# Performance work log

Hardware: AMD Instinct MI355X
Metric: run time of the kernel (lower is better)

## Reference

```python
import jax, jax.numpy as jnp
import numpy as np

B, T, D_IN, D_OUT = 32, 2048, 512, 512


def setup_inputs() -> dict:
    key = jax.random.key(0)
    k1, k2, k3 = jax.random.split(key, 3)
    x = jax.random.normal(k1, (B, T, D_IN), dtype=jnp.float32)
    # scale weights roughly like glorot / orthogonal init
    W = jax.random.normal(k2, (D_IN, D_OUT), dtype=jnp.float32) * (1.0 / np.sqrt(D_IN))
    W_recurrent = jax.random.normal(k3, (D_OUT, D_OUT), dtype=jnp.float32) * (1.0 / np.sqrt(D_OUT))
    b = jnp.zeros((D_OUT,), dtype=jnp.float32)
    return {"x": x, "W": W, "W_recurrent": W_recurrent, "b": b}


def reference(x, W, W_recurrent, b):
    # x: [B, T, D_in]. Vanilla RNN: h_t = tanh(x_t @ W + h_{t-1} @ W_rec + b)
    # Precompute input projections for all timesteps in one big GEMM,
    # then scan only the recurrent part (same math as per-step matmul).
    xw = jnp.einsum('bti,io->tbo', x, W) + b  # [T, B, D_out]
    h0 = jnp.zeros((x.shape[0], W.shape[1]), dtype=x.dtype)

    def step(h, xw_t):
        h_new = jnp.tanh(xw_t + h @ W_recurrent)
        return h_new, h_new

    _, states = jax.lax.scan(step, h0, xw)  # states: [T, B, D_out]
    # return_sequence=True -> [B, T, D_out]
    return jnp.transpose(states, (1, 0, 2))
```

## Files before the change

kernel.cpp:

```cpp
#include <hip/hip_runtime.h>

constexpr int B = 32, T = 2048, D = 512;

typedef float f32x4 __attribute__((ext_vector_type(4)));

__global__ __launch_bounds__(256) void xw_gemm(
    const float* __restrict__ A, const float* __restrict__ W,
    const float* __restrict__ bias, float* __restrict__ C) {
  __shared__ float As[16][68];
  __shared__ float Bs[16][68];
  const int tid = threadIdx.x;
  const int M0 = blockIdx.y * 64, N0 = blockIdx.x * 64;
  const int tn = tid & 15, tm = tid >> 4;
  const int rA = tid >> 2, kA = (tid & 3) << 2;
  const int kB = tid >> 4, nB = (tid & 15) << 2;
  float acc[4][4] = {};
  for (int k0 = 0; k0 < 512; k0 += 16) {
    float4 a4 = *(const float4*)&A[(size_t)(M0 + rA) * 512 + k0 + kA];
    As[kA + 0][rA] = a4.x;
    As[kA + 1][rA] = a4.y;
    As[kA + 2][rA] = a4.z;
    As[kA + 3][rA] = a4.w;
    *(float4*)&Bs[kB][nB] = *(const float4*)&W[(size_t)(k0 + kB) * 512 + N0 + nB];
    __syncthreads();
#pragma unroll
    for (int k = 0; k < 16; ++k) {
      float a0 = As[k][tm * 4 + 0], a1 = As[k][tm * 4 + 1];
      float a2 = As[k][tm * 4 + 2], a3 = As[k][tm * 4 + 3];
      float b0 = Bs[k][tn * 4 + 0], b1 = Bs[k][tn * 4 + 1];
      float b2 = Bs[k][tn * 4 + 2], b3 = Bs[k][tn * 4 + 3];
      acc[0][0] += a0 * b0; acc[0][1] += a0 * b1; acc[0][2] += a0 * b2; acc[0][3] += a0 * b3;
      acc[1][0] += a1 * b0; acc[1][1] += a1 * b1; acc[1][2] += a1 * b2; acc[1][3] += a1 * b3;
      acc[2][0] += a2 * b0; acc[2][1] += a2 * b1; acc[2][2] += a2 * b2; acc[2][3] += a2 * b3;
      acc[3][0] += a3 * b0; acc[3][1] += a3 * b1; acc[3][2] += a3 * b2; acc[3][3] += a3 * b3;
    }
    __syncthreads();
  }
#pragma unroll
  for (int i = 0; i < 4; ++i) {
    const size_t row = (size_t)(M0 + tm * 4 + i);
    float4 v;
    v.x = acc[i][0] + bias[N0 + tn * 4 + 0];
    v.y = acc[i][1] + bias[N0 + tn * 4 + 1];
    v.z = acc[i][2] + bias[N0 + tn * 4 + 2];
    v.w = acc[i][3] + bias[N0 + tn * 4 + 3];
    *(float4*)&C[row * 512 + N0 + tn * 4] = v;
  }
}

constexpr int NBLK = 256, NTHR = 512;

__device__ __forceinline__ float mytanh(float x) {
  const float xc = fminf(fmaxf(x, -9.0f), 9.0f);
  const float t = __builtin_amdgcn_exp2f(xc * 2.885390081777927f);
  return 1.0f - 2.0f / (t + 1.0f);
}

__device__ __forceinline__ void vld1(const float* p, float& v) {
  asm volatile("global_load_dword %0, %1, off sc1" : "+v"(v) : "v"(p) : "memory");
}
__device__ __forceinline__ void vld4(const float* p, f32x4& v) {
  asm volatile("global_load_dwordx4 %0, %1, off" : "=&v"(v) : "v"(p) : "memory");
}
__device__ __forceinline__ void vst4(float* p, f32x4 v) {
  asm volatile("global_store_dwordx4 %0, %1, off" ::"v"(p), "v"(v) : "memory");
}
__device__ __forceinline__ void vst4_sc1(float* p, f32x4 v) {
  asm volatile("global_store_dwordx4 %0, %1, off sc1" ::"v"(p), "v"(v) : "memory");
}

__global__ __launch_bounds__(NTHR)
__attribute__((amdgpu_waves_per_eu(2, 2)))
void rnn_scan(float* __restrict__ out, const float* __restrict__ Wrec,
              float* __restrict__ xbuf) {
  __shared__ float hs[2][512];
  const int blk = blockIdx.x;
  const int batch = blk >> 3;
  const int cg = blk & 7;
  const int tid = threadIdx.x;
  const int kq = tid & 31;
  const int cp = tid >> 5;
  const int k0 = kq * 16;
  const int col0 = cg * 64 + cp * 4;
  const int swz = (kq & 7) << 2;
  const int spos = tid ^ (((tid >> 4) & 7) << 2);
  const bool pub = (kq == 0);

  f32x4 wv[16];
#pragma unroll
  for (int i = 0; i < 16; ++i) vld4(&Wrec[(size_t)(k0 + i) * D + col0], wv[i]);
  asm volatile("s_waitcnt vmcnt(0)" ::: "memory");

  float* slab = xbuf + (size_t)batch * 1024;
  float* op = out + (size_t)batch * T * D;

  f32x4 xw4;
  float e = 1e30f;
  {
    f32x4 h0 = {0.f, 0.f, 0.f, 0.f};
    if (pub) {
      f32x4 x0;
      vld4(&op[col0], x0);
      asm volatile("s_waitcnt vmcnt(0)" : "+v"(x0)::"memory");
      h0[0] = mytanh(x0[0]); h0[1] = mytanh(x0[1]);
      h0[2] = mytanh(x0[2]); h0[3] = mytanh(x0[3]);
    }
    vld1(&slab[tid], e);
    if (pub) {
      vst4(&op[col0], h0);
      vst4_sc1(&slab[col0], h0 + 3.0f);
      vld4(&op[(size_t)1 * D + col0], xw4);
    }
  }

  for (int r = 1; r < T; ++r) {
    const int pv = (r - 1) & 1, pw = r & 1;
    const int iR = (r - 1) & 3, iW = r & 3;
    const float offR = ((iR & 1) ? 9.f : 3.f) * ((iR & 2) ? -1.f : 1.f);
    const float offW = ((iW & 1) ? 9.f : 3.f) * ((iW & 2) ? -1.f : 1.f);

    asm volatile("s_waitcnt vmcnt(3)" : "+v"(e)::"memory");
    __builtin_amdgcn_sched_barrier(0);
    if (fabsf(e - offR) >= 1.5f) {
      const float* pp = &slab[pv * 512 + tid];
      do {
        vld1(pp, e);
        asm volatile("s_waitcnt vmcnt(0)" : "+v"(e)::"memory");
        __builtin_amdgcn_sched_barrier(0);
      } while (fabsf(e - offR) >= 1.5f);
    }
    hs[pv][spos] = e - offR;
    __syncthreads();

    f32x4 a = {0.f, 0.f, 0.f, 0.f};
#pragma unroll
    for (int i4 = 0; i4 < 4; ++i4) {
      const f32x4 h4 = *(const f32x4*)&hs[pv][(k0 + 4 * i4) ^ swz];
#pragma unroll
      for (int j = 0; j < 4; ++j) {
        const float hh = h4[j];
        a[0] += wv[4 * i4 + j][0] * hh;
        a[1] += wv[4 * i4 + j][1] * hh;
        a[2] += wv[4 * i4 + j][2] * hh;
        a[3] += wv[4 * i4 + j][3] * hh;
      }
    }
#pragma unroll
    for (int m = 1; m < 32; m <<= 1) {
      a[0] += __shfl_xor(a[0], m);
      a[1] += __shfl_xor(a[1], m);
      a[2] += __shfl_xor(a[2], m);
      a[3] += __shfl_xor(a[3], m);
    }

    vld1(&slab[pw * 512 + tid], e);
    if (pub) {
      asm volatile("s_waitcnt vmcnt(1)" : "+v"(xw4)::"memory");
      f32x4 h;
      h[0] = mytanh(a[0] + xw4[0]);
      h[1] = mytanh(a[1] + xw4[1]);
      h[2] = mytanh(a[2] + xw4[2]);
      h[3] = mytanh(a[3] + xw4[3]);
      vst4(&op[(size_t)r * D + col0], h);
      vst4_sc1(&slab[pw * 512 + col0], h + offW);
      const int rn = (r + 1 < T) ? (r + 1) : r;
      vld4(&op[(size_t)rn * D + col0], xw4);
    }
  }
}

extern "C" void kernel_launch(void* const* d_in, const int* in_sizes, int n_in,
                              void* d_out, int out_size, void* d_ws, size_t ws_size,
                              hipStream_t stream) {
  const float* x = (const float*)d_in[0];
  const float* W = (const float*)d_in[1];
  const float* Wrec = (const float*)d_in[2];
  const float* bias = (const float*)d_in[3];
  float* out = (float*)d_out;

  xw_gemm<<<dim3(D / 64, (B * T) / 64), 256, 0, stream>>>(x, W, bias, out);

  hipMemsetAsync(d_ws, 0, 131072, stream);
  float* xbuf = (float*)d_ws;

  void* args[] = {(void*)&out, (void*)&Wrec, (void*)&xbuf};
  hipLaunchCooperativeKernel(reinterpret_cast<void*>(rnn_scan), dim3(NBLK),
                             dim3(NTHR), args, 0, stream);
}
```

Measured before the change: 5.120 ms.

## Poll hidden-state slab with one wave and replace block barrier with LDS flag

Only wave 0 now polls the cross-block hidden-state slab, using dwordx4 loads and a wave-wide all-check, then writes the state into LDS and raises a shared flag. The other waves spin on that flag instead of every thread polling and meeting at __syncthreads. Slab stores are reordered ahead of output stores. The aim is to cut per-step barrier cost and the number of polling loads on the serial recurrence critical path. The risks are LDS visibility ordering between waves, spin contention on the flag, and serialisation behind a single polling wave.

```diff
diff --git a/kernel.cpp b/kernel.cpp
--- a/kernel.cpp
+++ b/kernel.cpp
@@ -55,18 +55,21 @@
   const float t = __builtin_amdgcn_exp2f(xc * 2.885390081777927f);
   return 1.0f - 2.0f / (t + 1.0f);
 }
-
-__device__ __forceinline__ void vld1(const float* p, float& v) {
-  asm volatile("global_load_dword %0, %1, off sc1" : "+v"(v) : "v"(p) : "memory");
-}
-__device__ __forceinline__ void vld4(const float* p, f32x4& v) {
+__device__ __forceinline__ void ivld4_sc1(const float* p, f32x4& v) {
+  asm volatile("global_load_dwordx4 %0, %1, off sc1" : "=&v"(v) : "v"(p) : "memory");
+}
+__device__ __forceinline__ void ivld4(const float* p, f32x4& v) {
   asm volatile("global_load_dwordx4 %0, %1, off" : "=&v"(v) : "v"(p) : "memory");
 }
-__device__ __forceinline__ void vst4(float* p, f32x4 v) {
+__device__ __forceinline__ void ivst4(float* p, f32x4 v) {
   asm volatile("global_store_dwordx4 %0, %1, off" ::"v"(p), "v"(v) : "memory");
 }
-__device__ __forceinline__ void vst4_sc1(float* p, f32x4 v) {
+__device__ __forceinline__ void ivst4_sc1(float* p, f32x4 v) {
   asm volatile("global_store_dwordx4 %0, %1, off sc1" ::"v"(p), "v"(v) : "memory");
+}
+__device__ __forceinline__ int chk4(f32x4 v, float off) {
+  return (fabsf(v[0] - off) < 1.5f) & (fabsf(v[1] - off) < 1.5f) &
+         (fabsf(v[2] - off) < 1.5f) & (fabsf(v[3] - off) < 1.5f);
 }
 
 __global__ __launch_bounds__(NTHR)
@@ -74,42 +77,48 @@
 void rnn_scan(float* __restrict__ out, const float* __restrict__ Wrec,
               float* __restrict__ xbuf) {
   __shared__ float hs[2][512];
+  __shared__ int flag;
   const int blk = blockIdx.x;
-  const int batch = blk >> 3;
-  const int cg = blk & 7;
+  const int batch = blk >> 3, cg = blk & 7;
   const int tid = threadIdx.x;
-  const int kq = tid & 31;
-  const int cp = tid >> 5;
+  const int wvi = tid >> 6, lane = tid & 63;
+  const int kq = tid & 31, cp = tid >> 5;
   const int k0 = kq * 16;
   const int col0 = cg * 64 + cp * 4;
   const int swz = (kq & 7) << 2;
-  const int spos = tid ^ (((tid >> 4) & 7) << 2);
+  const bool w0 = (wvi == 0);
   const bool pub = (kq == 0);
 
-  f32x4 wv[16];
-#pragma unroll
-  for (int i = 0; i < 16; ++i) vld4(&Wrec[(size_t)(k0 + i) * D + col0], wv[i]);
+  if (tid == 0) flag = 0;
+  __syncthreads();
+
+  f32x4 wreg[16];
+#pragma unroll
+  for (int i = 0; i < 16; ++i) ivld4(&Wrec[(size_t)(k0 + i) * D + col0], wreg[i]);
   asm volatile("s_waitcnt vmcnt(0)" ::: "memory");
 
   float* slab = xbuf + (size_t)batch * 1024;
   float* op = out + (size_t)batch * T * D;
-
-  f32x4 xw4;
-  float e = 1e30f;
+  const int kA = 4 * lane, kB = 256 + 4 * lane;
+  const int iA = kA ^ (((kA >> 4) & 7) << 2);
+  const int iB = kB ^ (((kB >> 4) & 7) << 2);
+
+  f32x4 xw4 = {0, 0, 0, 0}, pA0, pA1;
   {
-    f32x4 h0 = {0.f, 0.f, 0.f, 0.f};
+    f32x4 h0 = {0, 0, 0, 0};
     if (pub) {
-      f32x4 x0;
-      vld4(&op[col0], x0);
-      asm volatile("s_waitcnt vmcnt(0)" : "+v"(x0)::"memory");
+      const f32x4 x0 = *(const f32x4*)&op[col0];
       h0[0] = mytanh(x0[0]); h0[1] = mytanh(x0[1]);
       h0[2] = mytanh(x0[2]); h0[3] = mytanh(x0[3]);
     }
-    vld1(&slab[tid], e);
+    if (w0) {
+      ivld4_sc1(&slab[kA], pA0);
+      ivld4_sc1(&slab[kB], pA1);
+    }
     if (pub) {
-      vst4(&op[col0], h0);
-      vst4_sc1(&slab[col0], h0 + 3.0f);
-      vld4(&op[(size_t)1 * D + col0], xw4);
+      ivst4_sc1(&slab[col0], h0 + 3.0f);
+      ivst4(&op[col0], h0);
+      ivld4(&op[(size_t)D + col0], xw4);
     }
   }
 
@@ -119,30 +128,43 @@
     const float offR = ((iR & 1) ? 9.f : 3.f) * ((iR & 2) ? -1.f : 1.f);
     const float offW = ((iW & 1) ? 9.f : 3.f) * ((iW & 2) ? -1.f : 1.f);
 
-    asm volatile("s_waitcnt vmcnt(3)" : "+v"(e)::"memory");
-    __builtin_amdgcn_sched_barrier(0);
-    if (fabsf(e - offR) >= 1.5f) {
-      const float* pp = &slab[pv * 512 + tid];
-      do {
-        vld1(pp, e);
-        asm volatile("s_waitcnt vmcnt(0)" : "+v"(e)::"memory");
-        __builtin_amdgcn_sched_barrier(0);
-      } while (fabsf(e - offR) >= 1.5f);
-    }
-    hs[pv][spos] = e - offR;
-    __syncthreads();
-
-    f32x4 a = {0.f, 0.f, 0.f, 0.f};
+    if (w0) {
+      asm volatile("s_waitcnt vmcnt(3)" : "+v"(pA0), "+v"(pA1)::"memory");
+      __builtin_amdgcn_sched_barrier(0);
+      int ok = chk4(pA0, offR) & chk4(pA1, offR);
+      if (!__all(ok)) {
+        const float* s0 = &slab[pv * 512 + kA];
+        const float* s1 = &slab[pv * 512 + kB];
+        do {
+          ivld4_sc1(s0, pA0);
+          ivld4_sc1(s1, pA1);
+          asm volatile("s_waitcnt vmcnt(0)" : "+v"(pA0), "+v"(pA1)::"memory");
+          __builtin_amdgcn_sched_barrier(0);
+          ok = chk4(pA0, offR) & chk4(pA1, offR);
+        } while (!__all(ok));
+      }
+      *(f32x4*)&hs[pv][iA] = pA0 - offR;
+      *(f32x4*)&hs[pv][iB] = pA1 - offR;
+      __threadfence_block();
+      if (lane == 0) *(volatile int*)&flag = r;
+      ivld4_sc1(&slab[pw * 512 + kA], pA0);
+      ivld4_sc1(&slab[pw * 512 + kB], pA1);
+    } else {
+      while (*(volatile int*)&flag < r) {}
+      __builtin_amdgcn_sched_barrier(0);
+    }
+
+    f32x4 a = {0, 0, 0, 0};
 #pragma unroll
     for (int i4 = 0; i4 < 4; ++i4) {
       const f32x4 h4 = *(const f32x4*)&hs[pv][(k0 + 4 * i4) ^ swz];
 #pragma unroll
       for (int j = 0; j < 4; ++j) {
         const float hh = h4[j];
-        a[0] += wv[4 * i4 + j][0] * hh;
-        a[1] += wv[4 * i4 + j][1] * hh;
-        a[2] += wv[4 * i4 + j][2] * hh;
-        a[3] += wv[4 * i4 + j][3] * hh;
+        a[0] += wreg[4 * i4 + j][0] * hh;
+        a[1] += wreg[4 * i4 + j][1] * hh;
+        a[2] += wreg[4 * i4 + j][2] * hh;
+        a[3] += wreg[4 * i4 + j][3] * hh;
       }
     }
 #pragma unroll
@@ -153,18 +175,21 @@
       a[3] += __shfl_xor(a[3], m);
     }
 
-    vld1(&slab[pw * 512 + tid], e);
     if (pub) {
-      asm volatile("s_waitcnt vmcnt(1)" : "+v"(xw4)::"memory");
+      if (w0)
+        asm volatile("s_waitcnt vmcnt(2)" : "+v"(xw4)::"memory");
+      else
+        asm volatile("s_waitcnt vmcnt(0)" : "+v"(xw4)::"memory");
+      __builtin_amdgcn_sched_barrier(0);
       f32x4 h;
       h[0] = mytanh(a[0] + xw4[0]);
       h[1] = mytanh(a[1] + xw4[1]);
       h[2] = mytanh(a[2] + xw4[2]);
       h[3] = mytanh(a[3] + xw4[3]);
-      vst4(&op[(size_t)r * D + col0], h);
-      vst4_sc1(&slab[pw * 512 + col0], h + offW);
+      ivst4_sc1(&slab[pw * 512 + col0], h + offW);
+      ivst4(&op[(size_t)r * D + col0], h);
       const int rn = (r + 1 < T) ? (r + 1) : r;
-      vld4(&op[(size_t)rn * D + col0], xw4);
+      ivld4(&op[(size_t)rn * D + col0], xw4);
     }
   }
 }
```

New measurement: 5.986 ms. 16.9% more time.
